# Performance work log

Measured on AMD Instinct MI355X. Metric: run time of the kernel, lower is better.

Reference implementation:

```python
import jax, jax.numpy as jnp
import numpy as np

B, T, C, H = 8, 1024, 1024, 16
D = C // H
EPS = 1e-5


def setup_inputs() -> dict:
    key = jax.random.key(0)
    ks = jax.random.split(key, 12)
    s = lambda k, shape, scale=0.02: jax.random.normal(k, shape, dtype=jnp.float32) * scale
    return {
        "x": jax.random.normal(ks[0], (B, T, C), dtype=jnp.float32),
        "ln1_w": jnp.ones((C,), jnp.float32),
        "ln1_b": jnp.zeros((C,), jnp.float32),
        "w_qkv": s(ks[1], (C, 3 * C)),
        "b_qkv": jnp.zeros((3 * C,), jnp.float32),
        "w_o": s(ks[2], (C, C)),
        "b_o": jnp.zeros((C,), jnp.float32),
        "ln2_w": jnp.ones((C,), jnp.float32),
        "ln2_b": jnp.zeros((C,), jnp.float32),
        "w_fc": s(ks[3], (C, 4 * C)),
        "b_fc": jnp.zeros((4 * C,), jnp.float32),
        "w_proj": s(ks[4], (4 * C, C)),
        "b_proj": jnp.zeros((C,), jnp.float32),
    }


def _layernorm(x, w, b):
    mu = jnp.mean(x, axis=-1, keepdims=True)
    var = jnp.mean(jnp.square(x - mu), axis=-1, keepdims=True)
    return (x - mu) * jax.lax.rsqrt(var + EPS) * w + b


def _attention(x, w_qkv, b_qkv, w_o, b_o):
    b, t, c = x.shape
    qkv = x @ w_qkv + b_qkv                      # [B,T,3C]
    q, k, v = jnp.split(qkv, 3, axis=-1)
    q = q.reshape(b, t, H, D)
    k = k.reshape(b, t, H, D)
    v = v.reshape(b, t, H, D)
    scores = jnp.einsum("bqhd,bkhd->bhqk", q, k) / jnp.sqrt(jnp.float32(D))
    mask = jnp.tril(jnp.ones((t, t), dtype=bool))  # causal
    scores = jnp.where(mask, scores, jnp.float32(-jnp.inf))
    att = jax.nn.softmax(scores, axis=-1)
    y = jnp.einsum("bhqk,bkhd->bqhd", att, v).reshape(b, t, c)
    return y @ w_o + b_o


def _mlp(x, w_fc, b_fc, w_proj, b_proj):
    h = jax.nn.gelu(x @ w_fc + b_fc, approximate=True)  # tanh GELU
    return h @ w_proj + b_proj


def reference(x, ln1_w, ln1_b, w_qkv, b_qkv, w_o, b_o, ln2_w, ln2_b, w_fc, b_fc, w_proj, b_proj):
    x = x + _attention(_layernorm(x, ln1_w, ln1_b), w_qkv, b_qkv, w_o, b_o)
    x = x + _mlp(_layernorm(x, ln2_w, ln2_b), w_fc, b_fc, w_proj, b_proj)
    return x
```

## Files before the change

kernel.cpp:

```cpp
#include <hip/hip_runtime.h>
#include <math.h>
#include <stdint.h>

typedef unsigned short u16;
typedef unsigned int u32;
typedef __attribute__((ext_vector_type(4))) unsigned short u16x4;
typedef __attribute__((ext_vector_type(8))) unsigned short u16x8;
typedef __attribute__((ext_vector_type(8))) __bf16 bf16x8;
typedef __attribute__((ext_vector_type(4))) float f32x4;

#define Bn 8
#define Tn 1024
#define Cn 1024
#define Hn 16
#define Dn 64
#define Mn 8192

#define F32_ONE_BITS 0x3F800000u

__device__ __forceinline__ float b2f(u16 u) {
  union { unsigned int i; float f; } v; v.i = ((unsigned int)u) << 16; return v.f;
}
__device__ __forceinline__ u16 f2b(float f) {
  union { float f; unsigned int i; } v; v.f = f;
  unsigned int r = v.i + 0x7fffu + ((v.i >> 16) & 1u);
  return (u16)(r >> 16);
}

__device__ __forceinline__ void async_ld16(const u16* g, u16* l) {
  __builtin_amdgcn_global_load_lds(
      (__attribute__((address_space(1))) void*)g,
      (__attribute__((address_space(3))) void*)l, 16, 0, 0);
}

__device__ __forceinline__ float gelu_fast(float x) {
  float u2 = 1.5957691216057308f * (x + 0.044715f * x * x * x);
  return x / (1.0f + __expf(-u2));
}

__global__ __launch_bounds__(256) void cvt_x_k(const void* __restrict__ src, u16* __restrict__ dst,
                                               const u32* __restrict__ flagp) {
  bool isf32 = (*flagp == F32_ONE_BITS);
  size_t i = ((size_t)blockIdx.x * 256 + threadIdx.x) * 4;
  if (isf32) {
    f32x4 v = *reinterpret_cast<const f32x4*>((const float*)src + i);
    u16x4 o;
#pragma unroll
    for (int j = 0; j < 4; j++) o[j] = f2b(v[j]);
    *reinterpret_cast<u16x4*>(dst + i) = o;
  } else {
    *reinterpret_cast<u16x4*>(dst + i) = *reinterpret_cast<const u16x4*>((const u16*)src + i);
  }
}

struct SmallCvt { const void* src[8]; u16* dst[8]; int n[8]; };

__global__ __launch_bounds__(256) void cvt_small_k(SmallCvt p, const u32* __restrict__ flagp) {
  bool isf32 = (*flagp == F32_ONE_BITS);
  int t = blockIdx.x * 256 + threadIdx.x;
  int off = 0;
#pragma unroll
  for (int i = 0; i < 8; i++) {
    int idx = t - off;
    if (idx >= 0 && idx < p.n[i]) {
      u16 v = isf32 ? f2b(((const float*)p.src[i])[idx]) : ((const u16*)p.src[i])[idx];
      p.dst[i][idx] = v;
    }
    off += p.n[i];
  }
}

__global__ __launch_bounds__(256) void transpose_k(const void* __restrict__ in,
                                                   u16* __restrict__ out, int K, int N,
                                                   const u32* __restrict__ flagp) {
  bool isf32 = (*flagp == F32_ONE_BITS);
  __shared__ u16 tile[32][33];
  int c0 = blockIdx.x * 32, r0 = blockIdx.y * 32;
  int tx = threadIdx.x, ty = threadIdx.y;
#pragma unroll
  for (int i = 0; i < 4; i++) {
    size_t idx = (size_t)(r0 + ty + i * 8) * N + c0 + tx;
    tile[ty + i * 8][tx] = isf32 ? f2b(((const float*)in)[idx]) : ((const u16*)in)[idx];
  }
  __syncthreads();
#pragma unroll
  for (int i = 0; i < 4; i++)
    out[(size_t)(c0 + ty + i * 8) * K + r0 + tx] = tile[tx][ty + i * 8];
}

__global__ __launch_bounds__(256) void ln_k(const u16* __restrict__ x, const u16* __restrict__ w,
                                            const u16* __restrict__ bi, u16* __restrict__ out) {
  int row = blockIdx.x, tid = threadIdx.x;
  const u16* xr = x + (size_t)row * Cn;
  u16x4 xv = *reinterpret_cast<const u16x4*>(xr + tid * 4);
  float v0 = b2f(xv[0]), v1 = b2f(xv[1]), v2 = b2f(xv[2]), v3 = b2f(xv[3]);
  float s = v0 + v1 + v2 + v3;
  float s2 = v0 * v0 + v1 * v1 + v2 * v2 + v3 * v3;
#pragma unroll
  for (int m = 1; m < 64; m <<= 1) {
    s += __shfl_xor(s, m, 64);
    s2 += __shfl_xor(s2, m, 64);
  }
  __shared__ float rs_[4], rs2_[4];
  int wave = tid >> 6, lane = tid & 63;
  if (lane == 0) { rs_[wave] = s; rs2_[wave] = s2; }
  __syncthreads();
  s = rs_[0] + rs_[1] + rs_[2] + rs_[3];
  s2 = rs2_[0] + rs2_[1] + rs2_[2] + rs2_[3];
  float mu = s * (1.0f / Cn);
  float var = s2 * (1.0f / Cn) - mu * mu;
  float rstd = rsqrtf(var + 1e-5f);
  u16x4 wv = *reinterpret_cast<const u16x4*>(w + tid * 4);
  u16x4 bv = *reinterpret_cast<const u16x4*>(bi + tid * 4);
  u16x4 ov;
  float vv[4] = {v0, v1, v2, v3};
#pragma unroll
  for (int j = 0; j < 4; j++)
    ov[j] = f2b((vv[j] - mu) * rstd * b2f(wv[j]) + b2f(bv[j]));
  *reinterpret_cast<u16x4*>(out + (size_t)row * Cn + tid * 4) = ov;
}

template <int GELU, int RES, int F32OUT>
__global__ __launch_bounds__(256) void gemm_k(const u16* __restrict__ A, const u16* __restrict__ BT,
                                              const u16* __restrict__ bias, const u16* __restrict__ res,
                                              void* __restrict__ Cout, int M, int N, int K) {
  __shared__ __align__(16) u16 As[128 * 64];
  __shared__ __align__(16) u16 Bs[128 * 64];
  int tid = threadIdx.x, wave = tid >> 6, lane = tid & 63;
  int l15 = lane & 15, quad = lane >> 4;
  int m0 = blockIdx.y * 128, n0 = blockIdx.x * 128;
  int wm = (wave & 1) * 64, wn = (wave >> 1) * 64;

  int offA[4][2], offB[4][2];
#pragma unroll
  for (int i = 0; i < 4; i++) {
    int rowA = wm + i * 16 + l15;
    int rowB = wn + i * 16 + l15;
#pragma unroll
    for (int kc = 0; kc < 2; kc++) {
      offA[i][kc] = rowA * 64 + (((kc * 4 + quad) ^ (rowA & 7)) * 8);
      offB[i][kc] = rowB * 64 + (((kc * 4 + quad) ^ (rowB & 7)) * 8);
    }
  }

  const u16 *aSrc[4], *bSrc[4];
  u16 *aDst[4], *bDst[4];
#pragma unroll
  for (int i = 0; i < 4; i++) {
    int c = wave * 256 + i * 64 + lane;
    int row = c >> 3;
    int j = (c & 7) ^ (row & 7);
    aSrc[i] = A + (size_t)(m0 + row) * K + j * 8;
    bSrc[i] = BT + (size_t)(n0 + row) * K + j * 8;
    aDst[i] = As + (size_t)c * 8;
    bDst[i] = Bs + (size_t)c * 8;
  }

  f32x4 acc[4][4];
#pragma unroll
  for (int mi = 0; mi < 4; mi++)
#pragma unroll
    for (int ni = 0; ni < 4; ni++) acc[mi][ni] = (f32x4){0.f, 0.f, 0.f, 0.f};

  for (int k0 = 0; k0 < K; k0 += 64) {
    __syncthreads();
#pragma unroll
    for (int i = 0; i < 4; i++) async_ld16(aSrc[i] + k0, aDst[i]);
#pragma unroll
    for (int i = 0; i < 4; i++) async_ld16(bSrc[i] + k0, bDst[i]);
    __syncthreads();
#pragma unroll
    for (int kc = 0; kc < 2; kc++) {
      bf16x8 av[4], bv[4];
#pragma unroll
      for (int i = 0; i < 4; i++) av[i] = *reinterpret_cast<const bf16x8*>(As + offA[i][kc]);
#pragma unroll
      for (int i = 0; i < 4; i++) bv[i] = *reinterpret_cast<const bf16x8*>(Bs + offB[i][kc]);
#pragma unroll
      for (int mi = 0; mi < 4; mi++)
#pragma unroll
        for (int ni = 0; ni < 4; ni++)
          acc[mi][ni] = __builtin_amdgcn_mfma_f32_16x16x32_bf16(av[mi], bv[ni], acc[mi][ni], 0, 0, 0);
    }
  }

#pragma unroll
  for (int ni = 0; ni < 4; ni++) {
    int col = n0 + wn + ni * 16 + l15;
    float bval = b2f(bias[col]);
#pragma unroll
    for (int mi = 0; mi < 4; mi++) {
#pragma unroll
      for (int r = 0; r < 4; r++) {
        int row = m0 + wm + mi * 16 + quad * 4 + r;
        float v = acc[mi][ni][r] + bval;
        if (GELU) v = gelu_fast(v);
        if (RES) v += b2f(res[(size_t)row * N + col]);
        if (F32OUT)
          ((float*)Cout)[(size_t)row * N + col] = v;
        else
          ((u16*)Cout)[(size_t)row * N + col] = f2b(v);
      }
    }
  }
}

__global__ __launch_bounds__(256) void attn_k(const u16* __restrict__ qkv, u16* __restrict__ y) {
  int qt = blockIdx.x, bh = blockIdx.y;
  int b = bh >> 4, h = bh & 15;
  int tid = threadIdx.x, wave = tid >> 6, lane = tid & 63;
  int l15 = lane & 15, quad = lane >> 4;

  __shared__ __align__(16) u16 Ks[64 * 72];
  __shared__ __align__(16) u16 VTs[64 * 72];
  __shared__ __align__(16) u16 Ps[4][16 * 72];

  const u16* base = qkv + (size_t)b * Tn * 3072 + h * 64;
  int q0 = qt * 64 + wave * 16;

  bf16x8 qfrag[2];
#pragma unroll
  for (int kc = 0; kc < 2; kc++)
    qfrag[kc] = *reinterpret_cast<const bf16x8*>(base + (size_t)(q0 + l15) * 3072 + kc * 32 + quad * 8);

  f32x4 o[4];
#pragma unroll
  for (int dn = 0; dn < 4; dn++) o[dn] = (f32x4){0.f, 0.f, 0.f, 0.f};
  float m_r[4] = {-1e30f, -1e30f, -1e30f, -1e30f};
  float l_r[4] = {0.f, 0.f, 0.f, 0.f};

  int kp = tid & 31, dgroup = tid >> 5;
  u32* vtw = reinterpret_cast<u32*>(VTs);

  int kvend = qt * 64;
  for (int kv0 = 0; kv0 <= kvend; kv0 += 64) {
    __syncthreads();
    {
      int key = tid >> 2, d0 = (tid & 3) * 16;
      const u16* kpt = base + 1024 + (size_t)(kv0 + key) * 3072 + d0;
      u16x8 ka = *reinterpret_cast<const u16x8*>(kpt);
      u16x8 kb = *reinterpret_cast<const u16x8*>(kpt + 8);
      *reinterpret_cast<u16x8*>(&Ks[key * 72 + d0]) = ka;
      *reinterpret_cast<u16x8*>(&Ks[key * 72 + d0 + 8]) = kb;
      const u16* vp0 = base + 2048 + (size_t)(kv0 + 2 * kp) * 3072 + dgroup * 8;
      u16x8 va = *reinterpret_cast<const u16x8*>(vp0);
      u16x8 vb = *reinterpret_cast<const u16x8*>(vp0 + 3072);
#pragma unroll
      for (int i = 0; i < 8; i++)
        vtw[(dgroup * 8 + i) * 36 + kp] = (u32)va[i] | ((u32)vb[i] << 16);
    }
    __syncthreads();

    float sv[4][4];
#pragma unroll
    for (int ni = 0; ni < 4; ni++) {
      f32x4 z = (f32x4){0.f, 0.f, 0.f, 0.f};
#pragma unroll
      for (int kc = 0; kc < 2; kc++) {
        bf16x8 bfr = *reinterpret_cast<const bf16x8*>(&Ks[(ni * 16 + l15) * 72 + kc * 32 + quad * 8]);
        z = __builtin_amdgcn_mfma_f32_16x16x32_bf16(qfrag[kc], bfr, z, 0, 0, 0);
      }
#pragma unroll
      for (int r = 0; r < 4; r++) sv[ni][r] = z[r];
    }
    bool diag = (kv0 + 64 > q0);
#pragma unroll
    for (int ni = 0; ni < 4; ni++)
#pragma unroll
      for (int r = 0; r < 4; r++) {
        float v = sv[ni][r] * 0.125f;
        if (diag && (kv0 + ni * 16 + l15 > q0 + quad * 4 + r)) v = -1e30f;
        sv[ni][r] = v;
      }
    float mt[4], al[4], rs[4];
#pragma unroll
    for (int r = 0; r < 4; r++) {
      mt[r] = fmaxf(fmaxf(sv[0][r], sv[1][r]), fmaxf(sv[2][r], sv[3][r]));
#pragma unroll
      for (int m = 1; m <= 8; m <<= 1) mt[r] = fmaxf(mt[r], __shfl_xor(mt[r], m, 64));
      float mn = fmaxf(m_r[r], mt[r]);
      al[r] = __expf(m_r[r] - mn);
      m_r[r] = mn;
      rs[r] = 0.f;
    }
#pragma unroll
    for (int ni = 0; ni < 4; ni++)
#pragma unroll
      for (int r = 0; r < 4; r++) {
        float p = __expf(sv[ni][r] - m_r[r]);
        sv[ni][r] = p;
        rs[r] += p;
      }
#pragma unroll
    for (int r = 0; r < 4; r++) {
#pragma unroll
      for (int m = 1; m <= 8; m <<= 1) rs[r] += __shfl_xor(rs[r], m, 64);
      l_r[r] = l_r[r] * al[r] + rs[r];
    }
#pragma unroll
    for (int dn = 0; dn < 4; dn++)
#pragma unroll
      for (int r = 0; r < 4; r++) o[dn][r] *= al[r];
#pragma unroll
    for (int ni = 0; ni < 4; ni++)
#pragma unroll
      for (int r = 0; r < 4; r++)
        Ps[wave][(quad * 4 + r) * 72 + ni * 16 + l15] = f2b(sv[ni][r]);
#pragma unroll
    for (int kc = 0; kc < 2; kc++) {
      bf16x8 afr = *reinterpret_cast<const bf16x8*>(&Ps[wave][l15 * 72 + kc * 32 + quad * 8]);
#pragma unroll
      for (int dn = 0; dn < 4; dn++) {
        bf16x8 bfr = *reinterpret_cast<const bf16x8*>(&VTs[(dn * 16 + l15) * 72 + kc * 32 + quad * 8]);
        o[dn] = __builtin_amdgcn_mfma_f32_16x16x32_bf16(afr, bfr, o[dn], 0, 0, 0);
      }
    }
  }
#pragma unroll
  for (int r = 0; r < 4; r++) {
    float inv = 1.0f / l_r[r];
    int row = b * Tn + q0 + quad * 4 + r;
#pragma unroll
    for (int dn = 0; dn < 4; dn++)
      y[(size_t)row * Cn + h * 64 + dn * 16 + l15] = f2b(o[dn][r] * inv);
  }
}

extern "C" void kernel_launch(void* const* d_in, const int* in_sizes, int n_in,
                              void* d_out, int out_size, void* d_ws, size_t ws_size,
                              hipStream_t stream) {
  const void* x      = d_in[0];
  const void* ln1_w  = d_in[1];
  const void* ln1_b  = d_in[2];
  const void* w_qkv  = d_in[3];
  const void* b_qkv  = d_in[4];
  const void* w_o    = d_in[5];
  const void* b_o    = d_in[6];
  const void* ln2_w  = d_in[7];
  const void* ln2_b  = d_in[8];
  const void* w_fc   = d_in[9];
  const void* b_fc   = d_in[10];
  const void* w_proj = d_in[11];
  const void* b_proj = d_in[12];
  const u32* flagp = (const u32*)ln1_w;

  size_t off = 0;
  char* wsb = (char*)d_ws;
  auto alloc = [&](size_t bytes) {
    void* p = wsb + off;
    off += (bytes + 255) & ~(size_t)255;
    return (u16*)p;
  };
  u16* wqkvT  = alloc((size_t)3072 * 1024 * 2);
  u16* woT    = alloc((size_t)1024 * 1024 * 2);
  u16* wfcT   = alloc((size_t)4096 * 1024 * 2);
  u16* wprojT = alloc((size_t)1024 * 4096 * 2);
  u16* xb     = alloc((size_t)Mn * 1024 * 2);
  u16* sm     = alloc((size_t)16384 * 2);
  u16* xn     = alloc((size_t)Mn * 1024 * 2);
  u16* ybuf   = alloc((size_t)Mn * 1024 * 2);
  u16* x1     = alloc((size_t)Mn * 1024 * 2);
  u16* big    = alloc((size_t)Mn * 4096 * 2);
  u16* qkvbuf = big;
  u16* hbuf   = big;
  if (off > ws_size) return;

  u16* LW1 = sm;
  u16* LB1 = sm + 1024;
  u16* BQKV = sm + 2048;
  u16* BO  = sm + 5120;
  u16* LW2 = sm + 6144;
  u16* LB2 = sm + 7168;
  u16* BFC = sm + 8192;
  u16* BPJ = sm + 12288;

  SmallCvt sc;
  sc.src[0] = ln1_w;  sc.dst[0] = LW1;  sc.n[0] = 1024;
  sc.src[1] = ln1_b;  sc.dst[1] = LB1;  sc.n[1] = 1024;
  sc.src[2] = b_qkv;  sc.dst[2] = BQKV; sc.n[2] = 3072;
  sc.src[3] = b_o;    sc.dst[3] = BO;   sc.n[3] = 1024;
  sc.src[4] = ln2_w;  sc.dst[4] = LW2;  sc.n[4] = 1024;
  sc.src[5] = ln2_b;  sc.dst[5] = LB2;  sc.n[5] = 1024;
  sc.src[6] = b_fc;   sc.dst[6] = BFC;  sc.n[6] = 4096;
  sc.src[7] = b_proj; sc.dst[7] = BPJ;  sc.n[7] = 1024;

  hipLaunchKernelGGL(cvt_small_k, dim3(52), dim3(256), 0, stream, sc, flagp);
  hipLaunchKernelGGL(cvt_x_k, dim3(Mn * 1024 / 4 / 256), dim3(256), 0, stream, x, xb, flagp);

  dim3 tb(32, 8);
  hipLaunchKernelGGL(transpose_k, dim3(3072 / 32, 1024 / 32), tb, 0, stream, w_qkv, wqkvT, 1024, 3072, flagp);
  hipLaunchKernelGGL(transpose_k, dim3(1024 / 32, 1024 / 32), tb, 0, stream, w_o, woT, 1024, 1024, flagp);
  hipLaunchKernelGGL(transpose_k, dim3(4096 / 32, 1024 / 32), tb, 0, stream, w_fc, wfcT, 1024, 4096, flagp);
  hipLaunchKernelGGL(transpose_k, dim3(1024 / 32, 4096 / 32), tb, 0, stream, w_proj, wprojT, 4096, 1024, flagp);

  hipLaunchKernelGGL(ln_k, dim3(Mn), dim3(256), 0, stream, xb, LW1, LB1, xn);
  hipLaunchKernelGGL((gemm_k<0, 0, 0>), dim3(3072 / 128, Mn / 128), dim3(256), 0, stream,
                     xn, wqkvT, BQKV, (const u16*)nullptr, (void*)qkvbuf, Mn, 3072, 1024);
  hipLaunchKernelGGL(attn_k, dim3(Tn / 64, Bn * Hn), dim3(256), 0, stream, qkvbuf, ybuf);
  hipLaunchKernelGGL((gemm_k<0, 1, 0>), dim3(1024 / 128, Mn / 128), dim3(256), 0, stream,
                     ybuf, woT, BO, xb, (void*)x1, Mn, 1024, 1024);
  hipLaunchKernelGGL(ln_k, dim3(Mn), dim3(256), 0, stream, x1, LW2, LB2, xn);
  hipLaunchKernelGGL((gemm_k<1, 0, 0>), dim3(4096 / 128, Mn / 128), dim3(256), 0, stream,
                     xn, wfcT, BFC, (const u16*)nullptr, (void*)hbuf, Mn, 4096, 1024);
  hipLaunchKernelGGL((gemm_k<0, 1, 1>), dim3(1024 / 128, Mn / 128), dim3(256), 0, stream,
                     hbuf, wprojT, BPJ, x1, d_out, Mn, 1024, 4096);
}
```

Measured before the change: 570.1 us.

## Pair mirrored causal query tiles per attention block to balance work and reuse KV

Each attention block now handles two query tiles, tile i and tile 15-i, so every block does the same amount of causal work. The grid halves, and each K/V tile loaded into shared memory serves both query tiles while it is in range of the shorter one. This removes load imbalance across blocks and cuts K/V global loads. In exchange, register pressure roughly doubles for accumulators, launch bounds now request 4 blocks per CU, and there are fewer blocks to fill the GPU.

```diff
diff --git a/kernel.cpp b/kernel.cpp
--- a/kernel.cpp
+++ b/kernel.cpp
@@ -205,8 +205,9 @@
   }
 }
 
-__global__ __launch_bounds__(256) void attn_k(const u16* __restrict__ qkv, u16* __restrict__ y) {
-  int qt = blockIdx.x, bh = blockIdx.y;
+__global__ __launch_bounds__(256, 4) void attn_k(const u16* __restrict__ qkv, u16* __restrict__ y) {
+  int qtA = blockIdx.x, qtB = (Tn / 64 - 1) - qtA;
+  int bh = blockIdx.y;
   int b = bh >> 4, h = bh & 15;
   int tid = threadIdx.x, wave = tid >> 6, lane = tid & 63;
   int l15 = lane & 15, quad = lane >> 4;
@@ -216,24 +217,98 @@
   __shared__ __align__(16) u16 Ps[4][16 * 72];
 
   const u16* base = qkv + (size_t)b * Tn * 3072 + h * 64;
-  int q0 = qt * 64 + wave * 16;
-
-  bf16x8 qfrag[2];
-#pragma unroll
-  for (int kc = 0; kc < 2; kc++)
-    qfrag[kc] = *reinterpret_cast<const bf16x8*>(base + (size_t)(q0 + l15) * 3072 + kc * 32 + quad * 8);
-
-  f32x4 o[4];
-#pragma unroll
-  for (int dn = 0; dn < 4; dn++) o[dn] = (f32x4){0.f, 0.f, 0.f, 0.f};
-  float m_r[4] = {-1e30f, -1e30f, -1e30f, -1e30f};
-  float l_r[4] = {0.f, 0.f, 0.f, 0.f};
+  int qA0 = qtA * 64 + wave * 16;
+  int qB0 = qtB * 64 + wave * 16;
+
+  bf16x8 qfragA[2], qfragB[2];
+#pragma unroll
+  for (int kc = 0; kc < 2; kc++) {
+    qfragA[kc] = *reinterpret_cast<const bf16x8*>(base + (size_t)(qA0 + l15) * 3072 + kc * 32 + quad * 8);
+    qfragB[kc] = *reinterpret_cast<const bf16x8*>(base + (size_t)(qB0 + l15) * 3072 + kc * 32 + quad * 8);
+  }
+
+  f32x4 oA[4], oB[4];
+#pragma unroll
+  for (int dn = 0; dn < 4; dn++) {
+    oA[dn] = (f32x4){0.f, 0.f, 0.f, 0.f};
+    oB[dn] = (f32x4){0.f, 0.f, 0.f, 0.f};
+  }
+  float mA[4] = {-1e30f, -1e30f, -1e30f, -1e30f}, mB[4] = {-1e30f, -1e30f, -1e30f, -1e30f};
+  float lA[4] = {0.f, 0.f, 0.f, 0.f}, lB[4] = {0.f, 0.f, 0.f, 0.f};
 
   int kp = tid & 31, dgroup = tid >> 5;
   u32* vtw = reinterpret_cast<u32*>(VTs);
 
-  int kvend = qt * 64;
-  for (int kv0 = 0; kv0 <= kvend; kv0 += 64) {
+  auto tile_step = [&](int kv0, int q0, bf16x8 (&qfrag)[2], f32x4 (&o)[4], float (&m_r)[4],
+                       float (&l_r)[4]) {
+    float sv[4][4];
+#pragma unroll
+    for (int ni = 0; ni < 4; ni++) {
+      f32x4 z = (f32x4){0.f, 0.f, 0.f, 0.f};
+#pragma unroll
+      for (int kc = 0; kc < 2; kc++) {
+        bf16x8 bfr = *reinterpret_cast<const bf16x8*>(&Ks[(ni * 16 + l15) * 72 + kc * 32 + quad * 8]);
+        z = __builtin_amdgcn_mfma_f32_16x16x32_bf16(qfrag[kc], bfr, z, 0, 0, 0);
+      }
+#pragma unroll
+      for (int r = 0; r < 4; r++) sv[ni][r] = z[r];
+    }
+    bool diag = (kv0 + 64 > q0);
+#pragma unroll
+    for (int ni = 0; ni < 4; ni++)
+#pragma unroll
+      for (int r = 0; r < 4; r++) {
+        float v = sv[ni][r] * 0.125f;
+        if (diag && (kv0 + ni * 16 + l15 > q0 + quad * 4 + r)) v = -1e30f;
+        sv[ni][r] = v;
+      }
+    float mt[4], al[4], rs[4];
+#pragma unroll
+    for (int r = 0; r < 4; r++) {
+      mt[r] = fmaxf(fmaxf(sv[0][r], sv[1][r]), fmaxf(sv[2][r], sv[3][r]));
+#pragma unroll
+      for (int m = 1; m <= 8; m <<= 1) mt[r] = fmaxf(mt[r], __shfl_xor(mt[r], m, 64));
+      float mn = fmaxf(m_r[r], mt[r]);
+      al[r] = __expf(m_r[r] - mn);
+      m_r[r] = mn;
+      rs[r] = 0.f;
+    }
+#pragma unroll
+    for (int ni = 0; ni < 4; ni++)
+#pragma unroll
+      for (int r = 0; r < 4; r++) {
+        float p = __expf(sv[ni][r] - m_r[r]);
+        sv[ni][r] = p;
+        rs[r] += p;
+      }
+#pragma unroll
+    for (int r = 0; r < 4; r++) {
+#pragma unroll
+      for (int m = 1; m <= 8; m <<= 1) rs[r] += __shfl_xor(rs[r], m, 64);
+      l_r[r] = l_r[r] * al[r] + rs[r];
+    }
+#pragma unroll
+    for (int dn = 0; dn < 4; dn++)
+#pragma unroll
+      for (int r = 0; r < 4; r++) o[dn][r] *= al[r];
+#pragma unroll
+    for (int ni = 0; ni < 4; ni++)
+#pragma unroll
+      for (int r = 0; r < 4; r++)
+        Ps[wave][(quad * 4 + r) * 72 + ni * 16 + l15] = f2b(sv[ni][r]);
+#pragma unroll
+    for (int kc = 0; kc < 2; kc++) {
+      bf16x8 afr = *reinterpret_cast<const bf16x8*>(&Ps[wave][l15 * 72 + kc * 32 + quad * 8]);
+#pragma unroll
+      for (int dn = 0; dn < 4; dn++) {
+        bf16x8 bfr = *reinterpret_cast<const bf16x8*>(&VTs[(dn * 16 + l15) * 72 + kc * 32 + quad * 8]);
+        o[dn] = __builtin_amdgcn_mfma_f32_16x16x32_bf16(afr, bfr, o[dn], 0, 0, 0);
+      }
+    }
+  };
+
+  int kvendA = qtA * 64, kvendB = qtB * 64;
+  for (int kv0 = 0; kv0 <= kvendB; kv0 += 64) {
     __syncthreads();
     {
       int key = tid >> 2, d0 = (tid & 3) * 16;
@@ -251,78 +326,20 @@
     }
     __syncthreads();
 
-    float sv[4][4];
-#pragma unroll
-    for (int ni = 0; ni < 4; ni++) {
-      f32x4 z = (f32x4){0.f, 0.f, 0.f, 0.f};
-#pragma unroll
-      for (int kc = 0; kc < 2; kc++) {
-        bf16x8 bfr = *reinterpret_cast<const bf16x8*>(&Ks[(ni * 16 + l15) * 72 + kc * 32 + quad * 8]);
-        z = __builtin_amdgcn_mfma_f32_16x16x32_bf16(qfrag[kc], bfr, z, 0, 0, 0);
-      }
-#pragma unroll
-      for (int r = 0; r < 4; r++) sv[ni][r] = z[r];
-    }
-    bool diag = (kv0 + 64 > q0);
-#pragma unroll
-    for (int ni = 0; ni < 4; ni++)
-#pragma unroll
-      for (int r = 0; r < 4; r++) {
-        float v = sv[ni][r] * 0.125f;
-        if (diag && (kv0 + ni * 16 + l15 > q0 + quad * 4 + r)) v = -1e30f;
-        sv[ni][r] = v;
-      }
-    float mt[4], al[4], rs[4];
-#pragma unroll
-    for (int r = 0; r < 4; r++) {
-      mt[r] = fmaxf(fmaxf(sv[0][r], sv[1][r]), fmaxf(sv[2][r], sv[3][r]));
-#pragma unroll
-      for (int m = 1; m <= 8; m <<= 1) mt[r] = fmaxf(mt[r], __shfl_xor(mt[r], m, 64));
-      float mn = fmaxf(m_r[r], mt[r]);
-      al[r] = __expf(m_r[r] - mn);
-      m_r[r] = mn;
-      rs[r] = 0.f;
-    }
-#pragma unroll
-    for (int ni = 0; ni < 4; ni++)
-#pragma unroll
-      for (int r = 0; r < 4; r++) {
-        float p = __expf(sv[ni][r] - m_r[r]);
-        sv[ni][r] = p;
-        rs[r] += p;
-      }
-#pragma unroll
-    for (int r = 0; r < 4; r++) {
-#pragma unroll
-      for (int m = 1; m <= 8; m <<= 1) rs[r] += __shfl_xor(rs[r], m, 64);
-      l_r[r] = l_r[r] * al[r] + rs[r];
-    }
-#pragma unroll
-    for (int dn = 0; dn < 4; dn++)
-#pragma unroll
-      for (int r = 0; r < 4; r++) o[dn][r] *= al[r];
-#pragma unroll
-    for (int ni = 0; ni < 4; ni++)
-#pragma unroll
-      for (int r = 0; r < 4; r++)
-        Ps[wave][(quad * 4 + r) * 72 + ni * 16 + l15] = f2b(sv[ni][r]);
-#pragma unroll
-    for (int kc = 0; kc < 2; kc++) {
-      bf16x8 afr = *reinterpret_cast<const bf16x8*>(&Ps[wave][l15 * 72 + kc * 32 + quad * 8]);
-#pragma unroll
-      for (int dn = 0; dn < 4; dn++) {
-        bf16x8 bfr = *reinterpret_cast<const bf16x8*>(&VTs[(dn * 16 + l15) * 72 + kc * 32 + quad * 8]);
-        o[dn] = __builtin_amdgcn_mfma_f32_16x16x32_bf16(afr, bfr, o[dn], 0, 0, 0);
-      }
-    }
-  }
+    tile_step(kv0, qB0, qfragB, oB, mB, lB);
+    if (kv0 <= kvendA) tile_step(kv0, qA0, qfragA, oA, mA, lA);
+  }
+
 #pragma unroll
   for (int r = 0; r < 4; r++) {
-    float inv = 1.0f / l_r[r];
-    int row = b * Tn + q0 + quad * 4 + r;
-#pragma unroll
-    for (int dn = 0; dn < 4; dn++)
-      y[(size_t)row * Cn + h * 64 + dn * 16 + l15] = f2b(o[dn][r] * inv);
+    float invA = 1.0f / lA[r], invB = 1.0f / lB[r];
+    int rowA = b * Tn + qA0 + quad * 4 + r;
+    int rowB = b * Tn + qB0 + quad * 4 + r;
+#pragma unroll
+    for (int dn = 0; dn < 4; dn++) {
+      y[(size_t)rowA * Cn + h * 64 + dn * 16 + l15] = f2b(oA[dn][r] * invA);
+      y[(size_t)rowB * Cn + h * 64 + dn * 16 + l15] = f2b(oB[dn][r] * invB);
+    }
   }
 }
 
@@ -396,7 +413,7 @@
   hipLaunchKernelGGL(ln_k, dim3(Mn), dim3(256), 0, stream, xb, LW1, LB1, xn);
   hipLaunchKernelGGL((gemm_k<0, 0, 0>), dim3(3072 / 128, Mn / 128), dim3(256), 0, stream,
                      xn, wqkvT, BQKV, (const u16*)nullptr, (void*)qkvbuf, Mn, 3072, 1024);
-  hipLaunchKernelGGL(attn_k, dim3(Tn / 64, Bn * Hn), dim3(256), 0, stream, qkvbuf, ybuf);
+  hipLaunchKernelGGL(attn_k, dim3(Tn / 128, Bn * Hn), dim3(256), 0, stream, qkvbuf, ybuf);
   hipLaunchKernelGGL((gemm_k<0, 1, 0>), dim3(1024 / 128, Mn / 128), dim3(256), 0, stream,
                      ybuf, woT, BO, xb, (void*)x1, Mn, 1024, 1024);
   hipLaunchKernelGGL(ln_k, dim3(Mn), dim3(256), 0, stream, x1, LW2, LB2, xn);
```

New measurement: 585.5 us. 2.7% more time.
